# Kernel tuning notes

Measured on AMD Instinct MI355X. Metric: run time of the kernel, lower is better.

Reference implementation:

```python
import jax, jax.numpy as jnp
import numpy as np

B, N, W, H = 2, 2048, 1024, 16
HD = W // H  # head dim = 64
STD = 0.02


def setup_inputs() -> dict:
    key = jax.random.key(0)
    ks = jax.random.split(key, 8)
    x = jax.random.normal(ks[0], (B, N, W), dtype=jnp.float32)
    # weights stored [in, out] (transposed vs torch nn.Linear)
    qkv_w = jax.random.normal(ks[1], (W, 3 * W), dtype=jnp.float32) * STD
    qkv_b = jnp.zeros((3 * W,), jnp.float32)
    proj_w = jax.random.normal(ks[2], (W, W), dtype=jnp.float32) * STD
    proj_b = jnp.zeros((W,), jnp.float32)
    fc_w = jax.random.normal(ks[3], (W, 4 * W), dtype=jnp.float32) * STD
    fc_b = jnp.zeros((4 * W,), jnp.float32)
    fc2_w = jax.random.normal(ks[4], (4 * W, W), dtype=jnp.float32) * STD
    fc2_b = jnp.zeros((W,), jnp.float32)
    ln1_g = jnp.ones((W,), jnp.float32)
    ln1_b = jnp.zeros((W,), jnp.float32)
    ln2_g = jnp.ones((W,), jnp.float32)
    ln2_b = jnp.zeros((W,), jnp.float32)
    return dict(x=x, ln1_g=ln1_g, ln1_b=ln1_b, qkv_w=qkv_w, qkv_b=qkv_b,
                proj_w=proj_w, proj_b=proj_b, ln2_g=ln2_g, ln2_b=ln2_b,
                fc_w=fc_w, fc_b=fc_b, fc2_w=fc2_w, fc2_b=fc2_b)


def _layernorm(x, g, b, eps=1e-5):
    mu = jnp.mean(x, axis=-1, keepdims=True)
    var = jnp.var(x, axis=-1, keepdims=True)
    return (x - mu) * jax.lax.rsqrt(var + eps) * g + b


def _attention(x, qkv_w, qkv_b, proj_w, proj_b):
    bs, n, w = x.shape
    qkv = x @ qkv_w + qkv_b                      # [b, n, 3W]
    qkv = qkv.reshape(bs, n, H, 3 * HD)
    q, k, v = jnp.split(qkv, 3, axis=-1)         # each [b, n, h, hd]
    scale = 1.0 / np.sqrt(np.sqrt(HD)).astype(np.float32)
    # hand-rolled attention: full [b, h, t, s] score matrix, fp32 softmax
    weight = jnp.einsum('bthc,bshc->bhts', q * scale, k * scale)
    weight = jax.nn.softmax(weight.astype(jnp.float32), axis=-1).astype(weight.dtype)
    out = jnp.einsum('bhts,bshc->bthc', weight, v).reshape(bs, n, w)
    return out @ proj_w + proj_b


def reference(x, ln1_g, ln1_b, qkv_w, qkv_b, proj_w, proj_b,
              ln2_g, ln2_b, fc_w, fc_b, fc2_w, fc2_b):
    x = x + _attention(_layernorm(x, ln1_g, ln1_b), qkv_w, qkv_b, proj_w, proj_b)
    h = _layernorm(x, ln2_g, ln2_b)
    h = jax.nn.gelu(h @ fc_w + fc_b, approximate=False) @ fc2_w + fc2_b
    return x + h
```

## Files before the change

### kernel.cpp

```cpp
#include <hip/hip_runtime.h>
#include <hip/hip_bf16.h>
#include <type_traits>
#include <cstdint>

using bf16 = __hip_bfloat16;
typedef __attribute__((ext_vector_type(8))) short bf16x8;
typedef __attribute__((ext_vector_type(4))) float f32x4;

__device__ __forceinline__ float bf2f(unsigned short u) {
    union { unsigned int i; float f; } c; c.i = ((unsigned int)u) << 16; return c.f;
}

#define GLLDS16(gp, lp)                                                          \
    __builtin_amdgcn_global_load_lds(                                            \
        (const __attribute__((address_space(1))) void*)(gp),                     \
        (__attribute__((address_space(3))) void*)(lp), 16, 0, 0)

__global__ __launch_bounds__(256) void transpose_f2b(const float* __restrict__ w,
                                                     bf16* __restrict__ wt,
                                                     int K, int N) {
    __shared__ bf16 t[32][33];
    const int tid = threadIdx.x;
    const int n0 = blockIdx.x * 32, k0 = blockIdx.y * 32;
#pragma unroll
    for (int i = 0; i < 4; ++i) {
        int idx = tid + i * 256;
        int r = idx >> 5, c = idx & 31;
        t[r][c] = __float2bfloat16(w[(size_t)(k0 + r) * N + n0 + c]);
    }
    __syncthreads();
#pragma unroll
    for (int i = 0; i < 4; ++i) {
        int idx = tid + i * 256;
        int r = idx >> 5, c = idx & 31;
        wt[(size_t)(n0 + r) * K + k0 + c] = t[c][r];
    }
}

__global__ __launch_bounds__(256) void vtrans_kernel(const bf16* __restrict__ qkv,
                                                     bf16* __restrict__ vtg) {
    __shared__ bf16 t[32][33];
    const int tid = threadIdx.x;
    const int s0 = blockIdx.x * 32, c0 = blockIdx.y * 32;
    const int bh = blockIdx.z, b = bh >> 4, h = bh & 15;
#pragma unroll
    for (int i = 0; i < 4; ++i) {
        int idx = tid + i * 256;
        int r = idx >> 5, c = idx & 31;
        t[r][c] = qkv[(size_t)(b * 2048 + s0 + r) * 3072 + h * 192 + 128 + c0 + c];
    }
    __syncthreads();
#pragma unroll
    for (int i = 0; i < 4; ++i) {
        int idx = tid + i * 256;
        int r = idx >> 5, c = idx & 31;
        vtg[((size_t)bh * 64 + c0 + r) * 2048 + s0 + c] = t[c][r];
    }
}

template <typename InT>
__global__ __launch_bounds__(256) void ln_kernel(const InT* __restrict__ x,
                                                 const float* __restrict__ g,
                                                 const float* __restrict__ bta,
                                                 bf16* __restrict__ y) {
    const int row = blockIdx.x, tid = threadIdx.x;
    const size_t base = (size_t)row * 1024 + tid * 4;
    float v[4];
    if constexpr (std::is_same_v<InT, float>) {
        float4 f = *(const float4*)(x + base);
        v[0] = f.x; v[1] = f.y; v[2] = f.z; v[3] = f.w;
    } else {
        ushort4 u = *(const ushort4*)((const unsigned short*)x + base);
        v[0] = bf2f(u.x); v[1] = bf2f(u.y); v[2] = bf2f(u.z); v[3] = bf2f(u.w);
    }
    float s = v[0] + v[1] + v[2] + v[3];
    float sq = v[0]*v[0] + v[1]*v[1] + v[2]*v[2] + v[3]*v[3];
#pragma unroll
    for (int off = 32; off > 0; off >>= 1) {
        s  += __shfl_down(s, off);
        sq += __shfl_down(sq, off);
    }
    __shared__ float red[8];
    const int wave = tid >> 6, lane = tid & 63;
    if (lane == 0) { red[wave] = s; red[4 + wave] = sq; }
    __syncthreads();
    s  = red[0] + red[1] + red[2] + red[3];
    sq = red[4] + red[5] + red[6] + red[7];
    const float mu   = s * (1.0f / 1024.0f);
    const float var  = sq * (1.0f / 1024.0f) - mu * mu;
    const float rstd = rsqrtf(var + 1e-5f);
#pragma unroll
    for (int e = 0; e < 4; ++e) {
        int col = tid * 4 + e;
        float yy = (v[e] - mu) * rstd * g[col] + bta[col];
        y[base + e] = __float2bfloat16(yy);
    }
}

template <int EPI, int BM>
__global__ __launch_bounds__(256) void gemm_kernel(const bf16* __restrict__ A,
                                                   const bf16* __restrict__ Bt,
                                                   const float* __restrict__ bias,
                                                   const void* __restrict__ resid,
                                                   void* __restrict__ Cout,
                                                   int M, int N, int K) {
    constexpr int IF = 4;
    constexpr int JF = (BM == 128) ? 4 : 2;
    __shared__ bf16 As[BM][72];
    __shared__ bf16 Bs[128][72];
    const int tid  = threadIdx.x;
    const int wave = tid >> 6, lane = tid & 63;
    const int quad = lane >> 4, l16 = lane & 15;
    const int wm = (BM == 128) ? (wave >> 1) * 64 : 0;
    const int wn = (BM == 128) ? (wave & 1) * 64 : wave * 32;
    const int bm = blockIdx.y * BM, bn = blockIdx.x * 128;

    f32x4 acc[IF][JF];
#pragma unroll
    for (int i = 0; i < IF; ++i)
#pragma unroll
        for (int j = 0; j < JF; ++j) acc[i][j] = (f32x4){0.f, 0.f, 0.f, 0.f};

    for (int kt = 0; kt < K; kt += 64) {
        __syncthreads();
#pragma unroll
        for (int i = 0; i < BM * 8 / 256; ++i) {
            int c0 = tid + i * 256;
            int r = c0 >> 3, kc = (c0 & 7) << 3;
            *(uint4*)(&As[r][kc]) = *(const uint4*)(A + (size_t)(bm + r) * K + kt + kc);
        }
#pragma unroll
        for (int i = 0; i < 4; ++i) {
            int c0 = tid + i * 256;
            int r = c0 >> 3, kc = (c0 & 7) << 3;
            *(uint4*)(&Bs[r][kc]) = *(const uint4*)(Bt + (size_t)(bn + r) * K + kt + kc);
        }
        __syncthreads();
#pragma unroll
        for (int ks = 0; ks < 2; ++ks) {
            bf16x8 af[IF], bfr[JF];
#pragma unroll
            for (int i = 0; i < IF; ++i)
                af[i] = *(const bf16x8*)(&As[wm + i * 16 + l16][ks * 32 + quad * 8]);
#pragma unroll
            for (int j = 0; j < JF; ++j)
                bfr[j] = *(const bf16x8*)(&Bs[wn + j * 16 + l16][ks * 32 + quad * 8]);
#pragma unroll
            for (int i = 0; i < IF; ++i)
#pragma unroll
                for (int j = 0; j < JF; ++j)
                    acc[i][j] = __builtin_amdgcn_mfma_f32_16x16x32_bf16(af[i], bfr[j], acc[i][j], 0, 0, 0);
        }
    }
#pragma unroll
    for (int i = 0; i < IF; ++i) {
#pragma unroll
        for (int j = 0; j < JF; ++j) {
#pragma unroll
            for (int r = 0; r < 4; ++r) {
                const int row = bm + wm + i * 16 + quad * 4 + r;
                const int col = bn + wn + j * 16 + l16;
                float v = acc[i][j][r] + bias[col];
                if constexpr (EPI == 1)
                    v = 0.5f * v * (1.0f + erff(v * 0.70710678118654752f));
                if constexpr (EPI == 2) {
                    v += ((const float*)resid)[(size_t)row * N + col];
                    ((bf16*)Cout)[(size_t)row * N + col] = __float2bfloat16(v);
                } else if constexpr (EPI == 3) {
                    v += bf2f(((const unsigned short*)resid)[(size_t)row * N + col]);
                    ((float*)Cout)[(size_t)row * N + col] = v;
                } else {
                    ((bf16*)Cout)[(size_t)row * N + col] = __float2bfloat16(v);
                }
            }
        }
    }
}

__global__ __launch_bounds__(256) void attn_kernel(const bf16* __restrict__ qkv,
                                                   const bf16* __restrict__ vtg,
                                                   bf16* __restrict__ Opart,
                                                   float* __restrict__ Lp) {
    __shared__ __align__(16) bf16 Ks[64 * 64];
    __shared__ __align__(16) bf16 Vs[64 * 64];
    __shared__ __align__(16) bf16 Ps[4][2][16][72];
    const int tid  = threadIdx.x;
    const int wave = tid >> 6, lane = tid & 63;
    const int quad = lane >> 4, l16 = lane & 15;
    const int qt = blockIdx.x, h = blockIdx.y;
    const int b = blockIdx.z >> 1, seg = blockIdx.z & 1;
    const size_t tok0 = (size_t)b * 2048;
    const int qbase = qt * 128 + wave * 32;

    bf16x8 qf[2][2];
#pragma unroll
    for (int set = 0; set < 2; ++set) {
        const bf16* qp = qkv + (tok0 + qbase + set * 16 + l16) * 3072 + h * 192 + quad * 8;
        qf[set][0] = *(const bf16x8*)(qp);
        qf[set][1] = *(const bf16x8*)(qp + 32);
    }

    const bf16* kg = qkv + (tok0 + (tid >> 3)) * 3072 + h * 192 + 64 + (tid & 7) * 8;
    const bf16* vg = vtg + ((size_t)(b * 16 + h) * 64 + (tid >> 3)) * 2048 + (tid & 7) * 8;

    const short oneb = 0x3f80;
    const bf16x8 ones = {oneb, oneb, oneb, oneb, oneb, oneb, oneb, oneb};

    f32x4 o[2][4], l_acc[2];
#pragma unroll
    for (int set = 0; set < 2; ++set) {
        l_acc[set] = (f32x4){0.f, 0.f, 0.f, 0.f};
#pragma unroll
        for (int j = 0; j < 4; ++j) o[set][j] = (f32x4){0.f, 0.f, 0.f, 0.f};
    }

    const int kt0 = seg * 1024;
    for (int kt = kt0; kt < kt0 + 1024; kt += 64) {
        __syncthreads();
        GLLDS16(kg + (size_t)kt * 3072,        &Ks[(wave * 64) * 8]);
        GLLDS16(kg + (size_t)(kt + 32) * 3072, &Ks[(wave * 64 + 256) * 8]);
        GLLDS16(vg + kt,                       &Vs[(wave * 64) * 8]);
        GLLDS16(vg + kt + 32 * 2048,           &Vs[(wave * 64 + 256) * 8]);
        __syncthreads();

#pragma unroll
        for (int j = 0; j < 4; ++j) {
            bf16x8 kb0 = *(const bf16x8*)(&Ks[(j * 16 + l16) * 64 + quad * 8]);
            bf16x8 kb1 = *(const bf16x8*)(&Ks[(j * 16 + l16) * 64 + 32 + quad * 8]);
#pragma unroll
            for (int set = 0; set < 2; ++set) {
                f32x4 s4 = (f32x4){0.f, 0.f, 0.f, 0.f};
                s4 = __builtin_amdgcn_mfma_f32_16x16x32_bf16(qf[set][0], kb0, s4, 0, 0, 0);
                s4 = __builtin_amdgcn_mfma_f32_16x16x32_bf16(qf[set][1], kb1, s4, 0, 0, 0);
#pragma unroll
                for (int r = 0; r < 4; ++r)
                    Ps[wave][set][quad * 4 + r][j * 16 + l16] =
                        __float2bfloat16(__expf(s4[r] * 0.125f));
            }
        }
#pragma unroll
        for (int kk = 0; kk < 2; ++kk) {
            bf16x8 pf0 = *(const bf16x8*)(&Ps[wave][0][l16][kk * 32 + quad * 8]);
            bf16x8 pf1 = *(const bf16x8*)(&Ps[wave][1][l16][kk * 32 + quad * 8]);
            l_acc[0] = __builtin_amdgcn_mfma_f32_16x16x32_bf16(pf0, ones, l_acc[0], 0, 0, 0);
            l_acc[1] = __builtin_amdgcn_mfma_f32_16x16x32_bf16(pf1, ones, l_acc[1], 0, 0, 0);
#pragma unroll
            for (int j = 0; j < 4; ++j) {
                bf16x8 vf = *(const bf16x8*)(&Vs[(j * 16 + l16) * 64 + kk * 32 + quad * 8]);
                o[0][j] = __builtin_amdgcn_mfma_f32_16x16x32_bf16(pf0, vf, o[0][j], 0, 0, 0);
                o[1][j] = __builtin_amdgcn_mfma_f32_16x16x32_bf16(pf1, vf, o[1][j], 0, 0, 0);
            }
        }
    }
    const size_t segoff = (size_t)seg * 4096;
#pragma unroll
    for (int set = 0; set < 2; ++set)
#pragma unroll
        for (int j = 0; j < 4; ++j)
#pragma unroll
            for (int r = 0; r < 4; ++r) {
                int row = qbase + set * 16 + quad * 4 + r;
                Opart[(segoff + tok0 + row) * 1024 + h * 64 + j * 16 + l16] =
                    __float2bfloat16(o[set][j][r]);
            }
    if (l16 == 0) {
#pragma unroll
        for (int set = 0; set < 2; ++set)
#pragma unroll
            for (int r = 0; r < 4; ++r) {
                int row = qbase + set * 16 + quad * 4 + r;
                Lp[(segoff + tok0 + row) * 16 + h] = l_acc[set][r];
            }
    }
}

__global__ __launch_bounds__(256) void merge_kernel(const bf16* __restrict__ Opart,
                                                    const float* __restrict__ Lp,
                                                    bf16* __restrict__ outp) {
    const int idx = blockIdx.x * 256 + threadIdx.x;
    const int c4 = idx & 15, h = (idx >> 4) & 15, gt = idx >> 8;
    const size_t li0 = (size_t)gt * 16 + h, li1 = li0 + 4096 * 16;
    float inv = 1.0f / (Lp[li0] + Lp[li1]);
    const size_t off = (size_t)gt * 1024 + h * 64 + c4 * 4;
    ushort4 a = *(const ushort4*)((const unsigned short*)Opart + off);
    ushort4 bb = *(const ushort4*)((const unsigned short*)Opart + off + (size_t)4096 * 1024);
    float va[4] = {bf2f(a.x), bf2f(a.y), bf2f(a.z), bf2f(a.w)};
    float vb[4] = {bf2f(bb.x), bf2f(bb.y), bf2f(bb.z), bf2f(bb.w)};
    unsigned short res[4];
#pragma unroll
    for (int e = 0; e < 4; ++e) {
        bf16 o = __float2bfloat16((va[e] + vb[e]) * inv);
        res[e] = *(unsigned short*)&o;
    }
    *(ushort4*)((unsigned short*)outp + off) = make_ushort4(res[0], res[1], res[2], res[3]);
}

extern "C" void kernel_launch(void* const* d_in, const int* in_sizes, int n_in,
                              void* d_out, int out_size, void* d_ws, size_t ws_size,
                              hipStream_t stream) {
    const float* x      = (const float*)d_in[0];
    const float* ln1_g  = (const float*)d_in[1];
    const float* ln1_b  = (const float*)d_in[2];
    const float* qkv_w  = (const float*)d_in[3];
    const float* qkv_b  = (const float*)d_in[4];
    const float* proj_w = (const float*)d_in[5];
    const float* proj_b = (const float*)d_in[6];
    const float* ln2_g  = (const float*)d_in[7];
    const float* ln2_b  = (const float*)d_in[8];
    const float* fc_w   = (const float*)d_in[9];
    const float* fc_b   = (const float*)d_in[10];
    const float* fc2_w  = (const float*)d_in[11];
    const float* fc2_b  = (const float*)d_in[12];
    float* outp = (float*)d_out;

    char* ws = (char*)d_ws;
    const size_t MB = 1024 * 1024;
    bf16*  wfcT   = (bf16*)(ws + 0 * MB);
    bf16*  lnbuf  = (bf16*)(ws + 8 * MB);
    bf16*  wprojT = (bf16*)(ws + 8 * MB);
    float* Lp     = (float*)(ws + 10 * MB);
    bf16*  wqkvT  = (bf16*)(ws + 16 * MB);
    bf16*  vtg    = (bf16*)(ws + 16 * MB);
    bf16*  attnout= (bf16*)(ws + 16 * MB);
    bf16*  fcact  = (bf16*)(ws + 16 * MB);
    bf16*  qkvb   = (bf16*)(ws + 24 * MB);
    bf16*  Opart  = (bf16*)(ws + 48 * MB);
    bf16*  wfc2T  = (bf16*)(ws + 48 * MB);
    bf16*  x1     = (bf16*)(ws + 56 * MB);

    transpose_f2b<<<dim3(96, 32),  256, 0, stream>>>(qkv_w, wqkvT, 1024, 3072);
    transpose_f2b<<<dim3(128, 32), 256, 0, stream>>>(fc_w,  wfcT,  1024, 4096);
    ln_kernel<float><<<4096, 256, 0, stream>>>(x, ln1_g, ln1_b, lnbuf);
    gemm_kernel<0, 128><<<dim3(24, 32), 256, 0, stream>>>(lnbuf, wqkvT, qkv_b, nullptr, qkvb, 4096, 3072, 1024);
    vtrans_kernel<<<dim3(64, 2, 32), 256, 0, stream>>>(qkvb, vtg);
    transpose_f2b<<<dim3(32, 32), 256, 0, stream>>>(proj_w, wprojT, 1024, 1024);
    attn_kernel<<<dim3(16, 16, 4), 256, 0, stream>>>(qkvb, vtg, Opart, Lp);
    merge_kernel<<<4096, 256, 0, stream>>>(Opart, Lp, attnout);
    transpose_f2b<<<dim3(32, 128), 256, 0, stream>>>(fc2_w, wfc2T, 4096, 1024);
    gemm_kernel<2, 64><<<dim3(8, 64), 256, 0, stream>>>(attnout, wprojT, proj_b, x, x1, 4096, 1024, 1024);
    ln_kernel<bf16><<<4096, 256, 0, stream>>>(x1, ln2_g, ln2_b, lnbuf);
    gemm_kernel<1, 128><<<dim3(32, 32), 256, 0, stream>>>(lnbuf, wfcT, fc_b, nullptr, fcact, 4096, 4096, 1024);
    gemm_kernel<3, 64><<<dim3(8, 64), 256, 0, stream>>>(fcact, wfc2T, fc2_b, x1, outp, 4096, 1024, 4096);
}
```

Baseline: 400.2 us.

## Prefetch next K tile into registers and split-K the fc2 GEMM

All GEMMs now load the next K tile from global memory into registers while the current tile's MFMAs run, hiding load latency. The fc2 GEMM is split into two K halves across blockIdx.z to double the number of blocks. The two bf16 partials are then combined with bias and residual in a new merge kernel. This adds extra memory traffic for the partials and loses some precision from rounding partial sums to bf16.

```diff
diff --git a/kernel.cpp b/kernel.cpp
--- a/kernel.cpp
+++ b/kernel.cpp
@@ -97,7 +97,7 @@
     }
 }
 
-template <int EPI, int BM>
+template <int EPI, int BM, int KSPLIT>
 __global__ __launch_bounds__(256) void gemm_kernel(const bf16* __restrict__ A,
                                                    const bf16* __restrict__ Bt,
                                                    const float* __restrict__ bias,
@@ -106,6 +106,7 @@
                                                    int M, int N, int K) {
     constexpr int IF = 4;
     constexpr int JF = (BM == 128) ? 4 : 2;
+    constexpr int APF = BM / 32;
     __shared__ bf16 As[BM][72];
     __shared__ bf16 Bs[128][72];
     const int tid  = threadIdx.x;
@@ -115,27 +116,53 @@
     const int wn = (BM == 128) ? (wave & 1) * 64 : wave * 32;
     const int bm = blockIdx.y * BM, bn = blockIdx.x * 128;
 
+    const int kseg = KSPLIT ? (K >> 1) : K;
+    const int k0   = KSPLIT ? blockIdx.z * kseg : 0;
+    const int k1   = k0 + kseg;
+
     f32x4 acc[IF][JF];
 #pragma unroll
     for (int i = 0; i < IF; ++i)
 #pragma unroll
         for (int j = 0; j < JF; ++j) acc[i][j] = (f32x4){0.f, 0.f, 0.f, 0.f};
 
-    for (int kt = 0; kt < K; kt += 64) {
+    uint4 pa[APF], pb[4];
+#pragma unroll
+    for (int i = 0; i < APF; ++i) {
+        int c0 = tid + i * 256, r = c0 >> 3, kc = (c0 & 7) << 3;
+        pa[i] = *(const uint4*)(A + (size_t)(bm + r) * K + k0 + kc);
+    }
+#pragma unroll
+    for (int i = 0; i < 4; ++i) {
+        int c0 = tid + i * 256, r = c0 >> 3, kc = (c0 & 7) << 3;
+        pb[i] = *(const uint4*)(Bt + (size_t)(bn + r) * K + k0 + kc);
+    }
+
+    for (int kt = k0; kt < k1; kt += 64) {
         __syncthreads();
 #pragma unroll
-        for (int i = 0; i < BM * 8 / 256; ++i) {
-            int c0 = tid + i * 256;
-            int r = c0 >> 3, kc = (c0 & 7) << 3;
-            *(uint4*)(&As[r][kc]) = *(const uint4*)(A + (size_t)(bm + r) * K + kt + kc);
+        for (int i = 0; i < APF; ++i) {
+            int c0 = tid + i * 256, r = c0 >> 3, kc = (c0 & 7) << 3;
+            *(uint4*)(&As[r][kc]) = pa[i];
         }
 #pragma unroll
         for (int i = 0; i < 4; ++i) {
-            int c0 = tid + i * 256;
-            int r = c0 >> 3, kc = (c0 & 7) << 3;
-            *(uint4*)(&Bs[r][kc]) = *(const uint4*)(Bt + (size_t)(bn + r) * K + kt + kc);
+            int c0 = tid + i * 256, r = c0 >> 3, kc = (c0 & 7) << 3;
+            *(uint4*)(&Bs[r][kc]) = pb[i];
         }
         __syncthreads();
+        if (kt + 64 < k1) {
+#pragma unroll
+            for (int i = 0; i < APF; ++i) {
+                int c0 = tid + i * 256, r = c0 >> 3, kc = (c0 & 7) << 3;
+                pa[i] = *(const uint4*)(A + (size_t)(bm + r) * K + kt + 64 + kc);
+            }
+#pragma unroll
+            for (int i = 0; i < 4; ++i) {
+                int c0 = tid + i * 256, r = c0 >> 3, kc = (c0 & 7) << 3;
+                pb[i] = *(const uint4*)(Bt + (size_t)(bn + r) * K + kt + 64 + kc);
+            }
+        }
 #pragma unroll
         for (int ks = 0; ks < 2; ++ks) {
             bf16x8 af[IF], bfr[JF];
@@ -160,21 +187,45 @@
             for (int r = 0; r < 4; ++r) {
                 const int row = bm + wm + i * 16 + quad * 4 + r;
                 const int col = bn + wn + j * 16 + l16;
-                float v = acc[i][j][r] + bias[col];
-                if constexpr (EPI == 1)
-                    v = 0.5f * v * (1.0f + erff(v * 0.70710678118654752f));
-                if constexpr (EPI == 2) {
-                    v += ((const float*)resid)[(size_t)row * N + col];
-                    ((bf16*)Cout)[(size_t)row * N + col] = __float2bfloat16(v);
-                } else if constexpr (EPI == 3) {
-                    v += bf2f(((const unsigned short*)resid)[(size_t)row * N + col]);
-                    ((float*)Cout)[(size_t)row * N + col] = v;
+                if constexpr (EPI == 4) {
+                    ((bf16*)Cout)[(size_t)blockIdx.z * M * N + (size_t)row * N + col] =
+                        __float2bfloat16(acc[i][j][r]);
                 } else {
-                    ((bf16*)Cout)[(size_t)row * N + col] = __float2bfloat16(v);
+                    float v = acc[i][j][r] + bias[col];
+                    if constexpr (EPI == 1)
+                        v = 0.5f * v * (1.0f + erff(v * 0.70710678118654752f));
+                    if constexpr (EPI == 2) {
+                        v += ((const float*)resid)[(size_t)row * N + col];
+                        ((bf16*)Cout)[(size_t)row * N + col] = __float2bfloat16(v);
+                    } else if constexpr (EPI == 3) {
+                        v += bf2f(((const unsigned short*)resid)[(size_t)row * N + col]);
+                        ((float*)Cout)[(size_t)row * N + col] = v;
+                    } else {
+                        ((bf16*)Cout)[(size_t)row * N + col] = __float2bfloat16(v);
+                    }
                 }
             }
         }
     }
+}
+
+__global__ __launch_bounds__(256) void fc2_merge_kernel(const bf16* __restrict__ part,
+                                                        const float* __restrict__ bias,
+                                                        const bf16* __restrict__ x1,
+                                                        float* __restrict__ outp) {
+    const int idx = blockIdx.x * 256 + threadIdx.x;
+    const int row = idx >> 8, col = (idx & 255) * 4;
+    const size_t off = (size_t)row * 1024 + col;
+    ushort4 a = *(const ushort4*)((const unsigned short*)part + off);
+    ushort4 b = *(const ushort4*)((const unsigned short*)part + off + (size_t)4096 * 1024);
+    ushort4 xr = *(const ushort4*)((const unsigned short*)x1 + off);
+    float4 bi = *(const float4*)(bias + col);
+    float4 o;
+    o.x = bf2f(a.x) + bf2f(b.x) + bi.x + bf2f(xr.x);
+    o.y = bf2f(a.y) + bf2f(b.y) + bi.y + bf2f(xr.y);
+    o.z = bf2f(a.z) + bf2f(b.z) + bi.z + bf2f(xr.z);
+    o.w = bf2f(a.w) + bf2f(b.w) + bi.w + bf2f(xr.w);
+    *(float4*)(outp + off) = o;
 }
 
 __global__ __launch_bounds__(256) void attn_kernel(const bf16* __restrict__ qkv,
@@ -315,30 +366,32 @@
 
     char* ws = (char*)d_ws;
     const size_t MB = 1024 * 1024;
-    bf16*  wfcT   = (bf16*)(ws + 0 * MB);
-    bf16*  lnbuf  = (bf16*)(ws + 8 * MB);
-    bf16*  wprojT = (bf16*)(ws + 8 * MB);
-    float* Lp     = (float*)(ws + 10 * MB);
-    bf16*  wqkvT  = (bf16*)(ws + 16 * MB);
-    bf16*  vtg    = (bf16*)(ws + 16 * MB);
-    bf16*  attnout= (bf16*)(ws + 16 * MB);
-    bf16*  fcact  = (bf16*)(ws + 16 * MB);
-    bf16*  qkvb   = (bf16*)(ws + 24 * MB);
-    bf16*  Opart  = (bf16*)(ws + 48 * MB);
-    bf16*  wfc2T  = (bf16*)(ws + 48 * MB);
-    bf16*  x1     = (bf16*)(ws + 56 * MB);
+    bf16*  wfcT    = (bf16*)(ws + 0 * MB);
+    bf16*  fc2part = (bf16*)(ws + 0 * MB);
+    bf16*  lnbuf   = (bf16*)(ws + 8 * MB);
+    bf16*  wprojT  = (bf16*)(ws + 8 * MB);
+    float* Lp      = (float*)(ws + 10 * MB);
+    bf16*  wqkvT   = (bf16*)(ws + 16 * MB);
+    bf16*  vtg     = (bf16*)(ws + 16 * MB);
+    bf16*  attnout = (bf16*)(ws + 16 * MB);
+    bf16*  fcact   = (bf16*)(ws + 16 * MB);
+    bf16*  qkvb    = (bf16*)(ws + 24 * MB);
+    bf16*  Opart   = (bf16*)(ws + 48 * MB);
+    bf16*  wfc2T   = (bf16*)(ws + 48 * MB);
+    bf16*  x1      = (bf16*)(ws + 56 * MB);
 
     transpose_f2b<<<dim3(96, 32),  256, 0, stream>>>(qkv_w, wqkvT, 1024, 3072);
     transpose_f2b<<<dim3(128, 32), 256, 0, stream>>>(fc_w,  wfcT,  1024, 4096);
     ln_kernel<float><<<4096, 256, 0, stream>>>(x, ln1_g, ln1_b, lnbuf);
-    gemm_kernel<0, 128><<<dim3(24, 32), 256, 0, stream>>>(lnbuf, wqkvT, qkv_b, nullptr, qkvb, 4096, 3072, 1024);
+    gemm_kernel<0, 128, 0><<<dim3(24, 32), 256, 0, stream>>>(lnbuf, wqkvT, qkv_b, nullptr, qkvb, 4096, 3072, 1024);
     vtrans_kernel<<<dim3(64, 2, 32), 256, 0, stream>>>(qkvb, vtg);
     transpose_f2b<<<dim3(32, 32), 256, 0, stream>>>(proj_w, wprojT, 1024, 1024);
     attn_kernel<<<dim3(16, 16, 4), 256, 0, stream>>>(qkvb, vtg, Opart, Lp);
     merge_kernel<<<4096, 256, 0, stream>>>(Opart, Lp, attnout);
     transpose_f2b<<<dim3(32, 128), 256, 0, stream>>>(fc2_w, wfc2T, 4096, 1024);
-    gemm_kernel<2, 64><<<dim3(8, 64), 256, 0, stream>>>(attnout, wprojT, proj_b, x, x1, 4096, 1024, 1024);
+    gemm_kernel<2, 64, 0><<<dim3(8, 64), 256, 0, stream>>>(attnout, wprojT, proj_b, x, x1, 4096, 1024, 1024);
     ln_kernel<bf16><<<4096, 256, 0, stream>>>(x1, ln2_g, ln2_b, lnbuf);
-    gemm_kernel<1, 128><<<dim3(32, 32), 256, 0, stream>>>(lnbuf, wfcT, fc_b, nullptr, fcact, 4096, 4096, 1024);
-    gemm_kernel<3, 64><<<dim3(8, 64), 256, 0, stream>>>(fcact, wfc2T, fc2_b, x1, outp, 4096, 1024, 4096);
-}
+    gemm_kernel<1, 128, 0><<<dim3(32, 32), 256, 0, stream>>>(lnbuf, wfcT, fc_b, nullptr, fcact, 4096, 4096, 1024);
+    gemm_kernel<4, 64, 1><<<dim3(8, 64, 2), 256, 0, stream>>>(fcact, wfc2T, nullptr, nullptr, fc2part, 4096, 1024, 4096);
+    fc2_merge_kernel<<<4096, 256, 0, stream>>>(fc2part, fc2_b, x1, outp);
+}
```

Result: slower. 770.0 us (+92.4%).
